# Kernel optimization log

Hardware: AMD Instinct MI355X
Metric: run time of the kernel (lower is better)

## Reference

```python
import jax, jax.numpy as jnp
import numpy as np

MAX_ITER = 50
N = 8192


def setup_inputs() -> dict:
    key = jax.random.key(0)
    M = jax.random.normal(key, (N, N), dtype=jnp.float32)
    return {"M": M}


def reference(M) -> jnp.ndarray:
    # Power iteration: v_{k+1} = (M v_k) / ||M v_k||_2, v_0 = ones(N)
    v0 = jnp.ones((M.shape[-1],), dtype=M.dtype)

    def step(v, _):
        res = M @ v
        v = res / jnp.linalg.norm(res)
        return v, None

    v, _ = jax.lax.scan(step, v0, None, length=MAX_ITER)
    return v
```

## Files before the change

kernel.cpp:

```cpp
#include <hip/hip_runtime.h>
#include <hip/hip_fp16.h>

#define N 8192
#define ITERS 50
#define ROWS 8

typedef unsigned int uint32;


__global__ void pi_init_kernel(float* __restrict__ bufA, float* __restrict__ nsq) {
    int i = blockIdx.x * blockDim.x + threadIdx.x;
    if (i < N) bufA[i] = 1.0f;
    if (i <= ITERS) nsq[i] = (i == 0) ? 1.0f : 0.0f;
}

__device__ __forceinline__ void pi_epilogue(float (&acc)[ROWS], int t, int row0,
                                            float s, float* __restrict__ vout,
                                            float* __restrict__ nsq_next) {
#pragma unroll
    for (int r = 0; r < ROWS; ++r) {
        float a = acc[r];
        for (int off = 32; off > 0; off >>= 1) a += __shfl_down(a, off, 64);
        acc[r] = a;
    }
    __shared__ float part[4][ROWS];
    const int wave = t >> 6, lane = t & 63;
    if (lane == 0) {
#pragma unroll
        for (int r = 0; r < ROWS; ++r) part[wave][r] = acc[r];
    }
    __syncthreads();
    float sq = 0.0f;
    if (t < ROWS) {
        const float sum = part[0][t] + part[1][t] + part[2][t] + part[3][t];
        const float y = sum * s;
        vout[row0 + t] = y;
        sq = y * y;
    }
    if (wave == 0) {
        for (int off = 32; off > 0; off >>= 1) sq += __shfl_down(sq, off, 64);
        if (lane == 0) atomicAdd(nsq_next, sq);
    }
}

__global__ __launch_bounds__(256) void pi_gemv_kernel(
        const float4* __restrict__ M4,
        const float4* __restrict__ vin4,
        float* __restrict__ vout,
        const float* __restrict__ nsq_prev,
        float* __restrict__ nsq_next) {
    const int t = threadIdx.x;
    const int row0 = blockIdx.x * ROWS;
    const float s = rsqrtf(*nsq_prev);
    constexpr int NV = N / 4;
    constexpr int CHUNKS = NV / 256;
    float acc[ROWS];
#pragma unroll
    for (int r = 0; r < ROWS; ++r) acc[r] = 0.0f;
    for (int c = 0; c < CHUNKS; ++c) {
        const int idx = c * 256 + t;
        const float4 vv = vin4[idx];
#pragma unroll
        for (int r = 0; r < ROWS; ++r) {
            const float4 m = M4[(size_t)(row0 + r) * NV + idx];
            acc[r] += m.x * vv.x + m.y * vv.y + m.z * vv.z + m.w * vv.w;
        }
    }
    pi_epilogue(acc, t, row0, s, vout, nsq_next);
}

__device__ __forceinline__ uint32 pack2h(float x, float y) {
    __half2 p = __float22half2_rn(make_float2(x, y));
    return *reinterpret_cast<uint32*>(&p);
}

__global__ __launch_bounds__(256) void pi_convert_kernel(
        const float4* __restrict__ M4,
        const float4* __restrict__ vin4,
        float* __restrict__ vout,
        const float* __restrict__ nsq_prev,
        float* __restrict__ nsq_next,
        uint4* __restrict__ h4) {
    const int row = blockIdx.x;
    const int t = threadIdx.x, w = t >> 6, l = t & 63;
    const float s = rsqrtf(*nsq_prev);
    const size_t rf = (size_t)row * (N / 4);
    const size_t rh = (size_t)row * (N / 8);
    float a = 0.0f;
#pragma unroll
    for (int half = 0; half < 2; ++half) {
        const int tile = w + 4 * half;
        float4 m[4];
#pragma unroll
        for (int j = 0; j < 4; ++j) m[j] = M4[rf + tile * 256 + 4 * l + j];
#pragma unroll
        for (int j = 0; j < 4; ++j) {
            const float4 vv = vin4[tile * 256 + 4 * l + j];
            a += m[j].x * vv.x + m[j].y * vv.y + m[j].z * vv.z + m[j].w * vv.w;
        }
        uint4 o0, o1;
        o0.x = pack2h(m[0].x, m[0].y);
        o0.y = pack2h(m[0].z, m[0].w);
        o0.z = pack2h(m[1].x, m[1].y);
        o0.w = pack2h(m[1].z, m[1].w);
        o1.x = pack2h(m[2].x, m[2].y);
        o1.y = pack2h(m[2].z, m[2].w);
        o1.z = pack2h(m[3].x, m[3].y);
        o1.w = pack2h(m[3].z, m[3].w);
        h4[rh + tile * 128 + 2 * l]     = o0;
        h4[rh + tile * 128 + 2 * l + 1] = o1;
    }
    for (int off = 32; off > 0; off >>= 1) a += __shfl_down(a, off, 64);
    __shared__ float part[4];
    if (l == 0) part[w] = a;
    __syncthreads();
    if (t == 0) {
        const float sum = part[0] + part[1] + part[2] + part[3];
        const float y = sum * s;
        vout[row] = y;
        atomicAdd(nsq_next, y * y);
    }
}

__device__ __forceinline__ float2 h2f(uint32 u) {
    __half2 h = *reinterpret_cast<__half2*>(&u);
    return __half22float2(h);
}

__global__ __launch_bounds__(256) void pi_gemv2h_kernel(
        const uint4* __restrict__ h4,
        const float4* __restrict__ vin4,
        float* __restrict__ vout,
        const float* __restrict__ nsq_prev,
        float* __restrict__ nsq_next) {
    const int t = threadIdx.x;
    const int row0 = blockIdx.x * ROWS;
    const float s = rsqrtf(*nsq_prev);
    float acc[ROWS];
#pragma unroll
    for (int r = 0; r < ROWS; ++r) acc[r] = 0.0f;
#pragma unroll
    for (int c = 0; c < 4; ++c) {
        const int idx = c * 256 + t;
        const float4 va = vin4[2 * idx];
        const float4 vb = vin4[2 * idx + 1];
#pragma unroll
        for (int r = 0; r < ROWS; ++r) {
            const uint4 h = h4[(size_t)(row0 + r) * 1024 + idx];
            const float2 f0 = h2f(h.x);
            const float2 f1 = h2f(h.y);
            const float2 f2 = h2f(h.z);
            const float2 f3 = h2f(h.w);
            acc[r] += f0.x * va.x + f0.y * va.y + f1.x * va.z + f1.y * va.w +
                      f2.x * vb.x + f2.y * vb.y + f3.x * vb.z + f3.y * vb.w;
        }
    }
    pi_epilogue(acc, t, row0, s, vout, nsq_next);
}

__global__ void pi_scale_kernel(const float* __restrict__ vin,
                                const float* __restrict__ nsq,
                                float* __restrict__ out) {
    int i = blockIdx.x * blockDim.x + threadIdx.x;
    const float s = rsqrtf(*nsq);
    if (i < N) out[i] = vin[i] * s;
}

extern "C" void kernel_launch(void* const* d_in, const int* in_sizes, int n_in,
                              void* d_out, int out_size, void* d_ws, size_t ws_size,
                              hipStream_t stream) {
    const float* M = (const float*)d_in[0];
    float* out = (float*)d_out;

    const size_t H_BYTES = (size_t)N * N * 2;
    const size_t VEC_BYTES = (size_t)(2 * N + ITERS + 1) * sizeof(float);
    const bool use2 = (ws_size >= H_BYTES + VEC_BYTES);

    char* ws = (char*)d_ws;
    float* bufA;
    float* bufB;
    float* nsq;
    uint4* h4 = nullptr;
    if (use2) {
        h4   = (uint4*)ws;
        bufA = (float*)(ws + H_BYTES);
        bufB = bufA + N;
        nsq  = bufB + N;
    } else {
        bufA = (float*)ws;
        bufB = bufA + N;
        nsq  = bufB + N;
    }

    pi_init_kernel<<<(N + 255) / 256, 256, 0, stream>>>(bufA, nsq);

    const float4* M4 = (const float4*)M;
    if (use2) {
        pi_convert_kernel<<<N, 256, 0, stream>>>(
            M4, (const float4*)bufA, bufB, nsq, nsq + 1, h4);
        for (int k = 2; k <= ITERS; ++k) {
            const float* vin = (k & 1) ? bufA : bufB;
            float* vout      = (k & 1) ? bufB : bufA;
            pi_gemv2h_kernel<<<N / ROWS, 256, 0, stream>>>(
                h4, (const float4*)vin, vout, nsq + (k - 1), nsq + k);
        }
    } else {
        for (int k = 1; k <= ITERS; ++k) {
            const float* vin = (k & 1) ? bufA : bufB;
            float* vout      = (k & 1) ? bufB : bufA;
            pi_gemv_kernel<<<N / ROWS, 256, 0, stream>>>(
                M4, (const float4*)vin, vout, nsq + (k - 1), nsq + k);
        }
    }
    pi_scale_kernel<<<(N + 255) / 256, 256, 0, stream>>>(bufA, nsq + ITERS, out);
}
```

Measured before the change: 1.572 ms.

## Stream fp16 matrix tiles into LDS with direct global-to-LDS loads and double buffering

Replaces the register-load fp16 GEMV with a kernel that uses global_load_lds to copy 16-byte chunks of the half-precision matrix straight into a double-buffered shared-memory tile. Each wave stages two rows per chunk while the previous chunk is consumed, with manual vmcnt/lgkmcnt waits and barriers. The input vector is preloaded into registers up front. The aim is deeper memory-level parallelism and overlap of loads with compute in a bandwidth-bound GEMV. In exchange it adds LDS traffic, barriers, and reliance on hand-tuned wait counts for correctness.

New measurement: 1.536 ms. 1.02x faster.

```diff
diff --git a/kernel.cpp b/kernel.cpp
--- a/kernel.cpp
+++ b/kernel.cpp
@@ -6,6 +6,13 @@
 #define ROWS 8
 
 typedef unsigned int uint32;
+
+#define AS1 __attribute__((address_space(1)))
+#define AS3 __attribute__((address_space(3)))
+
+__device__ __forceinline__ void gload_lds16(const void* g, void* l) {
+    __builtin_amdgcn_global_load_lds((const AS1 void*)g, (AS3 void*)l, 16, 0, 0);
+}
 
 
 __global__ void pi_init_kernel(float* __restrict__ bufA, float* __restrict__ nsq) {
@@ -127,34 +134,84 @@
     return __half22float2(h);
 }
 
-__global__ __launch_bounds__(256) void pi_gemv2h_kernel(
-        const uint4* __restrict__ h4,
+__global__ __launch_bounds__(256) void pi_gemv2h_lds_kernel(
+        const __half* __restrict__ hplane,
         const float4* __restrict__ vin4,
         float* __restrict__ vout,
         const float* __restrict__ nsq_prev,
         float* __restrict__ nsq_next) {
-    const int t = threadIdx.x;
+    __shared__ uint4 sbuf[2][ROWS][256];
+    const int t = threadIdx.x, w = t >> 6, l = t & 63;
     const int row0 = blockIdx.x * ROWS;
     const float s = rsqrtf(*nsq_prev);
+
+    float4 va[4], vb[4];
+#pragma unroll
+    for (int c = 0; c < 4; ++c) {
+        va[c] = vin4[2 * (c * 256 + t)];
+        vb[c] = vin4[2 * (c * 256 + t) + 1];
+    }
+    asm volatile("s_waitcnt vmcnt(0)" ::: "memory");
+
+    const __half* rowbase = hplane + (size_t)row0 * N;
     float acc[ROWS];
 #pragma unroll
     for (int r = 0; r < ROWS; ++r) acc[r] = 0.0f;
-#pragma unroll
-    for (int c = 0; c < 4; ++c) {
-        const int idx = c * 256 + t;
-        const float4 va = vin4[2 * idx];
-        const float4 vb = vin4[2 * idx + 1];
-#pragma unroll
-        for (int r = 0; r < ROWS; ++r) {
-            const uint4 h = h4[(size_t)(row0 + r) * 1024 + idx];
-            const float2 f0 = h2f(h.x);
-            const float2 f1 = h2f(h.y);
-            const float2 f2 = h2f(h.z);
-            const float2 f3 = h2f(h.w);
-            acc[r] += f0.x * va.x + f0.y * va.y + f1.x * va.z + f1.y * va.w +
-                      f2.x * vb.x + f2.y * vb.y + f3.x * vb.z + f3.y * vb.w;
-        }
-    }
+
+#define STAGE(c, b)                                                           \
+    {                                                                         \
+        _Pragma("unroll")                                                     \
+        for (int rr = 0; rr < 2; ++rr) {                                      \
+            const int r = 2 * w + rr;                                         \
+            const char* gb =                                                  \
+                (const char*)(rowbase + (size_t)r * N + (c) * 2048) + l * 16; \
+            _Pragma("unroll")                                                 \
+            for (int q = 0; q < 4; ++q) {                                     \
+                gload_lds16(gb + q * 1024, (void*)&sbuf[b][r][q * 64]);       \
+            }                                                                 \
+        }                                                                     \
+    }
+
+#define COMPUTE(c, b)                                                         \
+    {                                                                         \
+        _Pragma("unroll")                                                     \
+        for (int r = 0; r < ROWS; ++r) {                                      \
+            const uint4 h = sbuf[b][r][t];                                    \
+            const float2 f0 = h2f(h.x);                                       \
+            const float2 f1 = h2f(h.y);                                       \
+            const float2 f2 = h2f(h.z);                                       \
+            const float2 f3 = h2f(h.w);                                       \
+            acc[r] += f0.x * va[c].x + f0.y * va[c].y + f1.x * va[c].z +      \
+                      f1.y * va[c].w + f2.x * vb[c].x + f2.y * vb[c].y +      \
+                      f3.x * vb[c].z + f3.y * vb[c].w;                        \
+        }                                                                     \
+    }
+
+#define WAITV(n) asm volatile("s_waitcnt vmcnt(" #n ")" ::: "memory")
+#define WAITL    asm volatile("s_waitcnt lgkmcnt(0)" ::: "memory")
+#define BAR      __builtin_amdgcn_s_barrier(); asm volatile("" ::: "memory")
+
+    STAGE(0, 0)
+    STAGE(1, 1)
+    WAITV(8); BAR;
+    COMPUTE(0, 0)
+    WAITL; BAR;
+    STAGE(2, 0)
+    WAITV(8); BAR;
+    COMPUTE(1, 1)
+    WAITL; BAR;
+    STAGE(3, 1)
+    WAITV(8); BAR;
+    COMPUTE(2, 0)
+    WAITV(0); WAITL; BAR;
+    COMPUTE(3, 1)
+
+#undef STAGE
+#undef COMPUTE
+#undef WAITV
+#undef WAITL
+#undef BAR
+
     pi_epilogue(acc, t, row0, s, vout, nsq_next);
 }
 
@@ -201,8 +258,9 @@
         for (int k = 2; k <= ITERS; ++k) {
             const float* vin = (k & 1) ? bufA : bufB;
             float* vout      = (k & 1) ? bufB : bufA;
-            pi_gemv2h_kernel<<<N / ROWS, 256, 0, stream>>>(
-                h4, (const float4*)vin, vout, nsq + (k - 1), nsq + k);
+            pi_gemv2h_lds_kernel<<<N / ROWS, 256, 0, stream>>>(
+                (const __half*)h4, (const float4*)vin, vout,
+                nsq + (k - 1), nsq + k);
         }
     } else {
         for (int k = 1; k <= ITERS; ++k) {
```
